# Kernel optimization log

Measured on AMD Instinct MI355X. Metric: run time of the kernel, lower is better.

Reference implementation:

```python
import jax, jax.numpy as jnp
import numpy as np

MAX_MARKER = 16


def setup_inputs() -> dict:
    key = jax.random.key(0)
    ks = jax.random.split(key, 7)
    B, W, H = 65536, 512, 8
    s1 = 1.0 / np.sqrt(W)
    s2 = 1.0 / np.sqrt(H)
    return {
        "x": jax.random.normal(ks[0], (B, W), dtype=jnp.float32),
        "W1": jax.random.uniform(ks[1], (H, W), jnp.float32, -s1, s1),
        "b1": jax.random.uniform(ks[2], (H,), jnp.float32, -s1, s1),
        "W2": jax.random.uniform(ks[3], (H, H), jnp.float32, -s2, s2),
        "b2": jax.random.uniform(ks[4], (H,), jnp.float32, -s2, s2),
        "W3": jax.random.uniform(ks[5], (W, H), jnp.float32, -s2, s2),
        "b3": jax.random.uniform(ks[6], (W,), jnp.float32, -s2, s2),
    }


def reference(x, W1, b1, W2, b2, W3, b3):
    # tiny MLP: window -> 8 -> 8 -> window
    h = jax.nn.relu(x @ W1.T + b1)
    h = jax.nn.relu(h @ W2.T + b2)
    y = h @ W3.T + b3
    p = jax.nn.softmax(y, axis=1)
    # force endpoints on (x.data[:,0]=1; x.data[:,-1]=1)
    p = p.at[:, 0].set(1.0).at[:, -1].set(1.0)
    # top-k along dim 1; threshold = min of the top-k values per row
    top_vals, _ = jax.lax.top_k(p, MAX_MARKER)
    thr = top_vals[:, -1:]  # sorted desc -> last is min, shape [B,1]
    # binary mask writes: >= thr -> 1, else 0
    return jnp.where(p >= thr, 1.0, 0.0).astype(p.dtype)
```

## Files before the change

### kernel.cpp

```cpp
#include <hip/hip_runtime.h>
#include <math.h>

#define B_ROWS 65536
#define WDIM 512
#define HDIM 8
#define THREADS 512

typedef float native_float4 __attribute__((ext_vector_type(4)));

template<int CTRL, int ROWM>
__device__ __forceinline__ float dpp_mov(float oldv, float x) {
    return __int_as_float(__builtin_amdgcn_update_dpp(
        __float_as_int(oldv), __float_as_int(x), CTRL, ROWM, 0xF, false));
}

__device__ __forceinline__ float wave_sum(float x) {
    x += dpp_mov<0x121, 0xF>(0.f, x);
    x += dpp_mov<0x122, 0xF>(0.f, x);
    x += dpp_mov<0x124, 0xF>(0.f, x);
    x += dpp_mov<0x128, 0xF>(0.f, x);
    x += dpp_mov<0x142, 0xA>(0.f, x);
    x += dpp_mov<0x143, 0xC>(0.f, x);
    return __int_as_float(__builtin_amdgcn_readlane(__float_as_int(x), 63));
}

__device__ __forceinline__ float wave_max(float x) {
    x = fmaxf(x, dpp_mov<0x121, 0xF>(-INFINITY, x));
    x = fmaxf(x, dpp_mov<0x122, 0xF>(-INFINITY, x));
    x = fmaxf(x, dpp_mov<0x124, 0xF>(-INFINITY, x));
    x = fmaxf(x, dpp_mov<0x128, 0xF>(-INFINITY, x));
    x = fmaxf(x, dpp_mov<0x142, 0xA>(-INFINITY, x));
    x = fmaxf(x, dpp_mov<0x143, 0xC>(-INFINITY, x));
    return __int_as_float(__builtin_amdgcn_readlane(__float_as_int(x), 63));
}

__device__ __forceinline__ float dot8(native_float4 a0, native_float4 a1,
                                      native_float4 b0, native_float4 b1) {
    float s = a0.x * b0.x;
    s = fmaf(a0.y, b0.y, s); s = fmaf(a0.z, b0.z, s); s = fmaf(a0.w, b0.w, s);
    s = fmaf(a1.x, b1.x, s); s = fmaf(a1.y, b1.y, s);
    s = fmaf(a1.z, b1.z, s); s = fmaf(a1.w, b1.w, s);
    return s;
}

__global__ __launch_bounds__(THREADS, 2)
void fused_mlp_topk(const float* __restrict__ x,
                    const float* __restrict__ W1,
                    const float* __restrict__ b1,
                    const float* __restrict__ W2,
                    const float* __restrict__ b2,
                    const float* __restrict__ W3,
                    const float* __restrict__ b3,
                    float* __restrict__ out)
{
    __shared__ __align__(16) float sW1[HDIM * WDIM];
    __shared__ __align__(16) float sW3t[HDIM * WDIM];
    __shared__ __align__(16) float sb3[WDIM];

    const int tid = threadIdx.x;
    for (int i = tid; i < HDIM * WDIM; i += THREADS) sW1[i] = W1[i];
    for (int i = tid; i < HDIM * WDIM; i += THREADS) {
        int r = i >> 3, k = i & 7;
        sW3t[k * WDIM + r] = W3[i];
    }
    for (int i = tid; i < WDIM; i += THREADS) sb3[i] = b3[i];
    __syncthreads();

    const int lane = tid & 63;
    const int wave_id = blockIdx.x * (THREADS / 64) + (tid >> 6);

    const native_float4* sW1v = reinterpret_cast<const native_float4*>(sW1);
    const native_float4* sW3v = reinterpret_cast<const native_float4*>(sW3t);
    const native_float4* sb3v = reinterpret_cast<const native_float4*>(sb3);

    int ra = wave_id * 2;
    const native_float4* xpa = reinterpret_cast<const native_float4*>(x + (size_t)ra * WDIM);
    const native_float4* xpb = xpa + (WDIM / 4);
    native_float4 xa0 = __builtin_nontemporal_load(xpa + lane);
    native_float4 xa1 = __builtin_nontemporal_load(xpa + lane + 64);
    native_float4 xb0 = __builtin_nontemporal_load(xpb + lane);
    native_float4 xb1 = __builtin_nontemporal_load(xpb + lane + 64);

    #pragma unroll 1
    for (int it = 0; it < 4; ++it) {
        float pa[HDIM], pb[HDIM];
        #pragma unroll
        for (int j = 0; j < HDIM; ++j) {
            native_float4 w0 = sW1v[j * 128 + lane];
            native_float4 w1 = sW1v[j * 128 + lane + 64];
            pa[j] = dot8(xa0, xa1, w0, w1);
            pb[j] = dot8(xb0, xb1, w0, w1);
        }
        float h1a[HDIM], h1b[HDIM];
        #pragma unroll
        for (int j = 0; j < HDIM; ++j) {
            float sa = wave_sum(pa[j]) + b1[j];
            float sb = wave_sum(pb[j]) + b1[j];
            h1a[j] = sa > 0.f ? sa : 0.f;
            h1b[j] = sb > 0.f ? sb : 0.f;
        }

        float h2a[HDIM], h2b[HDIM];
        #pragma unroll
        for (int j = 0; j < HDIM; ++j) {
            float va = b2[j], vb = b2[j];
            #pragma unroll
            for (int k = 0; k < HDIM; ++k) {
                const float w = W2[j * HDIM + k];
                va = fmaf(w, h1a[k], va);
                vb = fmaf(w, h1b[k], vb);
            }
            h2a[j] = va > 0.f ? va : 0.f;
            h2b[j] = vb > 0.f ? vb : 0.f;
        }

        native_float4 ya0 = sb3v[lane];
        native_float4 ya1 = sb3v[lane + 64];
        native_float4 yb0 = ya0, yb1 = ya1;
        #pragma unroll
        for (int k = 0; k < HDIM; ++k) {
            const float ha = h2a[k], hb = h2b[k];
            native_float4 w0 = sW3v[k * 128 + lane];
            native_float4 w1 = sW3v[k * 128 + lane + 64];
            ya0 += ha * w0;  ya1 += ha * w1;
            yb0 += hb * w0;  yb1 += hb * w1;
        }

        const int nra = ra + 16384;
        native_float4 nxa0, nxa1, nxb0, nxb1;
        if (it < 3) {
            const native_float4* nxpa = reinterpret_cast<const native_float4*>(x + (size_t)nra * WDIM);
            const native_float4* nxpb = nxpa + (WDIM / 4);
            nxa0 = __builtin_nontemporal_load(nxpa + lane);
            nxa1 = __builtin_nontemporal_load(nxpa + lane + 64);
            nxb0 = __builtin_nontemporal_load(nxpb + lane);
            nxb1 = __builtin_nontemporal_load(nxpb + lane + 64);
        }

        float lma = fmaxf(fmaxf(fmaxf(ya0.x, ya0.y), fmaxf(ya0.z, ya0.w)),
                          fmaxf(fmaxf(ya1.x, ya1.y), fmaxf(ya1.z, ya1.w)));
        float lmb = fmaxf(fmaxf(fmaxf(yb0.x, yb0.y), fmaxf(yb0.z, yb0.w)),
                          fmaxf(fmaxf(yb1.x, yb1.y), fmaxf(yb1.z, yb1.w)));
        float ma = wave_max(lma);
        float mb = wave_max(lmb);

        float ea[8], eb[8];
        ea[0] = expf(ya0.x - ma); ea[1] = expf(ya0.y - ma);
        ea[2] = expf(ya0.z - ma); ea[3] = expf(ya0.w - ma);
        ea[4] = expf(ya1.x - ma); ea[5] = expf(ya1.y - ma);
        ea[6] = expf(ya1.z - ma); ea[7] = expf(ya1.w - ma);
        eb[0] = expf(yb0.x - mb); eb[1] = expf(yb0.y - mb);
        eb[2] = expf(yb0.z - mb); eb[3] = expf(yb0.w - mb);
        eb[4] = expf(yb1.x - mb); eb[5] = expf(yb1.y - mb);
        eb[6] = expf(yb1.z - mb); eb[7] = expf(yb1.w - mb);

        if (lane == 0)  { ea[0] = 0.f; eb[0] = 0.f; }
        if (lane == 63) { ea[7] = 0.f; eb[7] = 0.f; }

        unsigned Ua = 0x30000000u, Ub = 0x30000000u;
        for (int b = 27; b >= 0; --b) {
            const unsigned bit = 1u << b;
            const float cfa = __uint_as_float(Ua | bit);
            const float cfb = __uint_as_float(Ub | bit);
            int ca = 0, cb = 0;
            #pragma unroll
            for (int t = 0; t < 8; ++t) {
                ca += __popcll(__ballot(ea[t] > cfa));
                cb += __popcll(__ballot(eb[t] > cfb));
            }
            if (ca >= 14) Ua |= bit;
            if (cb >= 14) Ub |= bit;
        }
        const float thra = __uint_as_float(Ua + 1u);
        const float thrb = __uint_as_float(Ub + 1u);

        native_float4 r0, r1, q0, q1;
        r0.x = ea[0] >= thra ? 1.f : 0.f;  r0.y = ea[1] >= thra ? 1.f : 0.f;
        r0.z = ea[2] >= thra ? 1.f : 0.f;  r0.w = ea[3] >= thra ? 1.f : 0.f;
        r1.x = ea[4] >= thra ? 1.f : 0.f;  r1.y = ea[5] >= thra ? 1.f : 0.f;
        r1.z = ea[6] >= thra ? 1.f : 0.f;  r1.w = ea[7] >= thra ? 1.f : 0.f;
        q0.x = eb[0] >= thrb ? 1.f : 0.f;  q0.y = eb[1] >= thrb ? 1.f : 0.f;
        q0.z = eb[2] >= thrb ? 1.f : 0.f;  q0.w = eb[3] >= thrb ? 1.f : 0.f;
        q1.x = eb[4] >= thrb ? 1.f : 0.f;  q1.y = eb[5] >= thrb ? 1.f : 0.f;
        q1.z = eb[6] >= thrb ? 1.f : 0.f;  q1.w = eb[7] >= thrb ? 1.f : 0.f;
        if (lane == 0)  { r0.x = 1.f; q0.x = 1.f; }
        if (lane == 63) { r1.w = 1.f; q1.w = 1.f; }

        native_float4* oa = reinterpret_cast<native_float4*>(out + (size_t)ra * WDIM);
        native_float4* ob = oa + (WDIM / 4);
        __builtin_nontemporal_store(r0, oa + lane);
        __builtin_nontemporal_store(r1, oa + lane + 64);
        __builtin_nontemporal_store(q0, ob + lane);
        __builtin_nontemporal_store(q1, ob + lane + 64);

        ra = nra;
        xa0 = nxa0; xa1 = nxa1; xb0 = nxb0; xb1 = nxb1;
    }
}

extern "C" void kernel_launch(void* const* d_in, const int* in_sizes, int n_in,
                              void* d_out, int out_size, void* d_ws, size_t ws_size,
                              hipStream_t stream) {
    const float* x  = (const float*)d_in[0];
    const float* W1 = (const float*)d_in[1];
    const float* b1 = (const float*)d_in[2];
    const float* W2 = (const float*)d_in[3];
    const float* b2 = (const float*)d_in[4];
    const float* W3 = (const float*)d_in[5];
    const float* b3 = (const float*)d_in[6];
    float* out = (float*)d_out;

    fused_mlp_topk<<<dim3(1024), dim3(THREADS), 0, stream>>>(x, W1, b1, W2, b2, W3, b3, out);
}
```

Measured before the change: 348.2 us.

## Select top-k on order-preserving logit bits, drop softmax, use radix-4 search

Drops the softmax (wave max and exps), since exp is monotonic and top-k selection on the logits gives the same mask. The logits are mapped to order-preserving unsigned keys. The bitwise binary search becomes a 2-bit-per-step radix search over 32 bits: 16 rounds with 3 candidate thresholds each, instead of 28 rounds with one. This cuts exp work and the number of serial ballot rounds but adds more ballots per round. It also changes tie behaviour, because exact ties are now judged on the logits rather than on rounded probabilities.

```diff
diff --git a/kernel.cpp b/kernel.cpp
--- a/kernel.cpp
+++ b/kernel.cpp
@@ -24,16 +24,6 @@
     return __int_as_float(__builtin_amdgcn_readlane(__float_as_int(x), 63));
 }
 
-__device__ __forceinline__ float wave_max(float x) {
-    x = fmaxf(x, dpp_mov<0x121, 0xF>(-INFINITY, x));
-    x = fmaxf(x, dpp_mov<0x122, 0xF>(-INFINITY, x));
-    x = fmaxf(x, dpp_mov<0x124, 0xF>(-INFINITY, x));
-    x = fmaxf(x, dpp_mov<0x128, 0xF>(-INFINITY, x));
-    x = fmaxf(x, dpp_mov<0x142, 0xA>(-INFINITY, x));
-    x = fmaxf(x, dpp_mov<0x143, 0xC>(-INFINITY, x));
-    return __int_as_float(__builtin_amdgcn_readlane(__float_as_int(x), 63));
-}
-
 __device__ __forceinline__ float dot8(native_float4 a0, native_float4 a1,
                                       native_float4 b0, native_float4 b1) {
     float s = a0.x * b0.x;
@@ -41,6 +31,11 @@
     s = fmaf(a1.x, b1.x, s); s = fmaf(a1.y, b1.y, s);
     s = fmaf(a1.z, b1.z, s); s = fmaf(a1.w, b1.w, s);
     return s;
+}
+
+__device__ __forceinline__ unsigned ford(float f) {
+    unsigned b = __float_as_uint(f);
+    return b ^ ((unsigned)((int)b >> 31) | 0x80000000u);
 }
 
 __global__ __launch_bounds__(THREADS, 2)
@@ -137,52 +132,45 @@
             nxb1 = __builtin_nontemporal_load(nxpb + lane + 64);
         }
 
-        float lma = fmaxf(fmaxf(fmaxf(ya0.x, ya0.y), fmaxf(ya0.z, ya0.w)),
-                          fmaxf(fmaxf(ya1.x, ya1.y), fmaxf(ya1.z, ya1.w)));
-        float lmb = fmaxf(fmaxf(fmaxf(yb0.x, yb0.y), fmaxf(yb0.z, yb0.w)),
-                          fmaxf(fmaxf(yb1.x, yb1.y), fmaxf(yb1.z, yb1.w)));
-        float ma = wave_max(lma);
-        float mb = wave_max(lmb);
-
-        float ea[8], eb[8];
-        ea[0] = expf(ya0.x - ma); ea[1] = expf(ya0.y - ma);
-        ea[2] = expf(ya0.z - ma); ea[3] = expf(ya0.w - ma);
-        ea[4] = expf(ya1.x - ma); ea[5] = expf(ya1.y - ma);
-        ea[6] = expf(ya1.z - ma); ea[7] = expf(ya1.w - ma);
-        eb[0] = expf(yb0.x - mb); eb[1] = expf(yb0.y - mb);
-        eb[2] = expf(yb0.z - mb); eb[3] = expf(yb0.w - mb);
-        eb[4] = expf(yb1.x - mb); eb[5] = expf(yb1.y - mb);
-        eb[6] = expf(yb1.z - mb); eb[7] = expf(yb1.w - mb);
-
-        if (lane == 0)  { ea[0] = 0.f; eb[0] = 0.f; }
-        if (lane == 63) { ea[7] = 0.f; eb[7] = 0.f; }
-
-        unsigned Ua = 0x30000000u, Ub = 0x30000000u;
-        for (int b = 27; b >= 0; --b) {
-            const unsigned bit = 1u << b;
-            const float cfa = __uint_as_float(Ua | bit);
-            const float cfb = __uint_as_float(Ub | bit);
-            int ca = 0, cb = 0;
+        unsigned ua[8], ub[8];
+        ua[0] = ford(ya0.x); ua[1] = ford(ya0.y); ua[2] = ford(ya0.z); ua[3] = ford(ya0.w);
+        ua[4] = ford(ya1.x); ua[5] = ford(ya1.y); ua[6] = ford(ya1.z); ua[7] = ford(ya1.w);
+        ub[0] = ford(yb0.x); ub[1] = ford(yb0.y); ub[2] = ford(yb0.z); ub[3] = ford(yb0.w);
+        ub[4] = ford(yb1.x); ub[5] = ford(yb1.y); ub[6] = ford(yb1.z); ub[7] = ford(yb1.w);
+        if (lane == 0)  { ua[0] = 0u; ub[0] = 0u; }
+        if (lane == 63) { ua[7] = 0u; ub[7] = 0u; }
+
+        unsigned Ua = 0u, Ub = 0u;
+        for (int b = 30; b >= 0; b -= 2) {
+            const unsigned ca1 = Ua | (1u << b), ca2 = Ua | (2u << b), ca3 = Ua | (3u << b);
+            const unsigned cb1 = Ub | (1u << b), cb2 = Ub | (2u << b), cb3 = Ub | (3u << b);
+            int na1 = 0, na2 = 0, na3 = 0, nb1 = 0, nb2 = 0, nb3 = 0;
             #pragma unroll
             for (int t = 0; t < 8; ++t) {
-                ca += __popcll(__ballot(ea[t] > cfa));
-                cb += __popcll(__ballot(eb[t] > cfb));
+                na1 += __popcll(__ballot(ua[t] > ca1));
+                na2 += __popcll(__ballot(ua[t] > ca2));
+                na3 += __popcll(__ballot(ua[t] > ca3));
+                nb1 += __popcll(__ballot(ub[t] > cb1));
+                nb2 += __popcll(__ballot(ub[t] > cb2));
+                nb3 += __popcll(__ballot(ub[t] > cb3));
             }
-            if (ca >= 14) Ua |= bit;
-            if (cb >= 14) Ub |= bit;
-        }
-        const float thra = __uint_as_float(Ua + 1u);
-        const float thrb = __uint_as_float(Ub + 1u);
+            const unsigned da = (na3 >= 14) ? 3u : (na2 >= 14) ? 2u : (na1 >= 14) ? 1u : 0u;
+            const unsigned db = (nb3 >= 14) ? 3u : (nb2 >= 14) ? 2u : (nb1 >= 14) ? 1u : 0u;
+            Ua |= da << b;
+            Ub |= db << b;
+        }
+        const unsigned thra = Ua + 1u;
+        const unsigned thrb = Ub + 1u;
 
         native_float4 r0, r1, q0, q1;
-        r0.x = ea[0] >= thra ? 1.f : 0.f;  r0.y = ea[1] >= thra ? 1.f : 0.f;
-        r0.z = ea[2] >= thra ? 1.f : 0.f;  r0.w = ea[3] >= thra ? 1.f : 0.f;
-        r1.x = ea[4] >= thra ? 1.f : 0.f;  r1.y = ea[5] >= thra ? 1.f : 0.f;
-        r1.z = ea[6] >= thra ? 1.f : 0.f;  r1.w = ea[7] >= thra ? 1.f : 0.f;
-        q0.x = eb[0] >= thrb ? 1.f : 0.f;  q0.y = eb[1] >= thrb ? 1.f : 0.f;
-        q0.z = eb[2] >= thrb ? 1.f : 0.f;  q0.w = eb[3] >= thrb ? 1.f : 0.f;
-        q1.x = eb[4] >= thrb ? 1.f : 0.f;  q1.y = eb[5] >= thrb ? 1.f : 0.f;
-        q1.z = eb[6] >= thrb ? 1.f : 0.f;  q1.w = eb[7] >= thrb ? 1.f : 0.f;
+        r0.x = ua[0] >= thra ? 1.f : 0.f;  r0.y = ua[1] >= thra ? 1.f : 0.f;
+        r0.z = ua[2] >= thra ? 1.f : 0.f;  r0.w = ua[3] >= thra ? 1.f : 0.f;
+        r1.x = ua[4] >= thra ? 1.f : 0.f;  r1.y = ua[5] >= thra ? 1.f : 0.f;
+        r1.z = ua[6] >= thra ? 1.f : 0.f;  r1.w = ua[7] >= thra ? 1.f : 0.f;
+        q0.x = ub[0] >= thrb ? 1.f : 0.f;  q0.y = ub[1] >= thrb ? 1.f : 0.f;
+        q0.z = ub[2] >= thrb ? 1.f : 0.f;  q0.w = ub[3] >= thrb ? 1.f : 0.f;
+        q1.x = ub[4] >= thrb ? 1.f : 0.f;  q1.y = ub[5] >= thrb ? 1.f : 0.f;
+        q1.z = ub[6] >= thrb ? 1.f : 0.f;  q1.w = ub[7] >= thrb ? 1.f : 0.f;
         if (lane == 0)  { r0.x = 1.f; q0.x = 1.f; }
         if (lane == 63) { r1.w = 1.f; q1.w = 1.f; }
 
```

After: 407.6 us. 1.17x slower.
